# Optimization experiments

Measured on AMD Instinct MI355X. Metric: run time of the kernel, lower is better.

Reference implementation:

```python
import jax, jax.numpy as jnp
import numpy as np

D_MODEL = 512
NUM_HEADS = 8
BATCH = 2
SEQ = 2048


def setup_inputs() -> dict:
    key = jax.random.key(0)
    ks = jax.random.split(key, 10)
    H = D_MODEL * NUM_HEADS  # concat width = 4096
    scale_in = 1.0 / np.sqrt(D_MODEL)
    scale_h = 1.0 / np.sqrt(H)
    inp = {
        "input_data": jax.random.normal(ks[0], (BATCH, SEQ, D_MODEL), dtype=jnp.float32),
        # causal mask, broadcastable to [n, h, q, k]; masked_fill where mask == 0
        "mask": jnp.tril(jnp.ones((SEQ, SEQ), dtype=jnp.int32))[None, None, :, :],
        "Wq": jax.random.normal(ks[1], (D_MODEL, H), dtype=jnp.float32) * scale_in,
        "bq": jnp.zeros((H,), dtype=jnp.float32),
        "Wk": jax.random.normal(ks[2], (D_MODEL, H), dtype=jnp.float32) * scale_in,
        "bk": jnp.zeros((H,), dtype=jnp.float32),
        "Wv": jax.random.normal(ks[3], (D_MODEL, H), dtype=jnp.float32) * scale_in,
        "bv": jnp.zeros((H,), dtype=jnp.float32),
        "Wo": jax.random.normal(ks[4], (H, D_MODEL), dtype=jnp.float32) * scale_h,
        "bo": jnp.zeros((D_MODEL,), dtype=jnp.float32),
    }
    return inp


def reference(input_data, mask, Wq, bq, Wk, bk, Wv, bv, Wo, bo):
    n, s, d_model = input_data.shape
    H = Wq.shape[1] // d_model  # num_heads; per-head dim == d_model in this module
    q = (input_data @ Wq + bq).reshape(n, s, H, d_model)
    k = (input_data @ Wk + bk).reshape(n, s, H, d_model)
    v = (input_data @ Wv + bv).reshape(n, s, H, d_model)
    scores = jnp.einsum('nqhd,nkhd->nhqk', q, k) / jnp.sqrt(jnp.float32(d_model))
    scores = jnp.where(mask == 0, jnp.float32(-1e9), scores)
    weights = jax.nn.softmax(scores, axis=-1)
    # Faithful to source: contracts weights over BOTH k and q axes (source quirk)
    output = jnp.einsum('nhkq,nvhd->nvhd', weights, v)
    concat = output.reshape(n, s, H * d_model)
    return concat @ Wo + bo
```

## Files before the change

kernel.cpp:

```cpp
#include <hip/hip_runtime.h>


#define DM 512
#define HC 4096
#define SEQF 2048.0f

typedef short bf16x8 __attribute__((ext_vector_type(8)));
typedef float f32x4 __attribute__((ext_vector_type(4)));

#define LDR 40

__device__ __forceinline__ void split2(float x, ushort& h, ushort& l) {
    unsigned b = __float_as_uint(x);
    h = (ushort)(b >> 16);
    float hf = __uint_as_float((unsigned)(h) << 16);
    l = (ushort)(__float_as_uint(x - hf) >> 16);
}

template <int ROWS>
__device__ __forceinline__ void stage_f32(const float* __restrict__ src, int ld, int row0,
                                          int k0, ushort* Hh, ushort* Hl, int tid) {
    const int r   = (ROWS == 128) ? (tid >> 1) : (tid >> 2);
    const int co  = (ROWS == 128) ? ((tid & 1) * 16) : ((tid & 3) * 8);
    const int NF4 = (ROWS == 128) ? 4 : 2;
    const float* p = src + (size_t)(row0 + r) * ld + k0 + co;
#pragma unroll
    for (int c = 0; c < NF4; ++c) {
        float4 v = *reinterpret_cast<const float4*>(p + c * 4);
        ushort4 uh, ul;
        split2(v.x, uh.x, ul.x);
        split2(v.y, uh.y, ul.y);
        split2(v.z, uh.z, ul.z);
        split2(v.w, uh.w, ul.w);
        *reinterpret_cast<ushort4*>(&Hh[r * LDR + co + c * 4]) = uh;
        *reinterpret_cast<ushort4*>(&Hl[r * LDR + co + c * 4]) = ul;
    }
}

template <int ROWS>
__device__ __forceinline__ void stage_bf16(const ushort* __restrict__ srcH,
                                           const ushort* __restrict__ srcL, int ld, int row0,
                                           int k0, ushort* Hh, ushort* Hl, int tid) {
    const int r   = (ROWS == 128) ? (tid >> 1) : (tid >> 2);
    const int co  = (ROWS == 128) ? ((tid & 1) * 16) : ((tid & 3) * 8);
    const int NI4 = (ROWS == 128) ? 2 : 1;
    const size_t off = (size_t)(row0 + r) * ld + k0 + co;
#pragma unroll
    for (int c = 0; c < NI4; ++c) {
        *reinterpret_cast<int4*>(&Hh[r * LDR + co + c * 8]) =
            *reinterpret_cast<const int4*>(&srcH[off + c * 8]);
        *reinterpret_cast<int4*>(&Hl[r * LDR + co + c * 8]) =
            *reinterpret_cast<const int4*>(&srcL[off + c * 8]);
    }
}

__global__ __launch_bounds__(256) void prep_wo(const float* __restrict__ Wo,
                                               const float* __restrict__ bv,
                                               ushort* __restrict__ WoTh,
                                               ushort* __restrict__ WoTl,
                                               float* __restrict__ cvec) {
    __shared__ float T[64][65];
    const int bj = blockIdx.x;
    const int bn = blockIdx.y;
    const int tid = threadIdx.x;
    {
        const int r = tid >> 2, c16 = (tid & 3) * 16;
        const float* p = Wo + (size_t)(bj * 64 + r) * DM + bn * 64 + c16;
#pragma unroll
        for (int c = 0; c < 4; ++c) {
            float4 v = *reinterpret_cast<const float4*>(p + c * 4);
            T[r][c16 + c * 4 + 0] = v.x;
            T[r][c16 + c * 4 + 1] = v.y;
            T[r][c16 + c * 4 + 2] = v.z;
            T[r][c16 + c * 4 + 3] = v.w;
        }
    }
    __syncthreads();
    {
        const int rn = tid >> 2, c16 = (tid & 3) * 16;
        const size_t off = (size_t)(bn * 64 + rn) * HC + bj * 64 + c16;
#pragma unroll
        for (int q = 0; q < 4; ++q) {
            ushort4 uh, ul;
            split2(T[c16 + q * 4 + 0][rn], uh.x, ul.x);
            split2(T[c16 + q * 4 + 1][rn], uh.y, ul.y);
            split2(T[c16 + q * 4 + 2][rn], uh.z, ul.z);
            split2(T[c16 + q * 4 + 3][rn], uh.w, ul.w);
            *reinterpret_cast<ushort4*>(&WoTh[off + q * 4]) = uh;
            *reinterpret_cast<ushort4*>(&WoTl[off + q * 4]) = ul;
        }
    }
    if (tid < 64) {
        float s = 0.f;
#pragma unroll 8
        for (int j = 0; j < 64; ++j) s = fmaf(bv[bj * 64 + j], T[j][tid], s);
        atomicAdd(&cvec[bn * 64 + tid], SEQF * s);
    }
}

__global__ __launch_bounds__(256) void gemm_wcT(const ushort* __restrict__ WoTh,
                                                const ushort* __restrict__ WoTl,
                                                const float* __restrict__ Wv,
                                                float* __restrict__ WcT) {
    __shared__ ushort Ah[128 * LDR], Al[128 * LDR], Bh[128 * LDR], Bl[128 * LDR];
    const int d = blockIdx.x;
    const int lin = (d & 7) * 32 + (d >> 3);
    const int kc = lin >> 4, mt = (lin >> 2) & 3, nt = lin & 3;
    const int a0 = mt * 128, b0 = nt * 128, kbase = kc * 256;
    const int tid = threadIdx.x, wave = tid >> 6, lane = tid & 63;
    const int wm = (wave >> 1) * 64, wn = (wave & 1) * 64;
    const int fr = lane & 15, fs = (lane >> 4) * 8;

    f32x4 acc[4][4] = {};
    for (int t = 0; t < 8; ++t) {
        const int k0 = kbase + t * 32;
        stage_bf16<128>(WoTh, WoTl, HC, a0, k0, Ah, Al, tid);
        stage_f32<128>(Wv, HC, b0, k0, Bh, Bl, tid);
        __syncthreads();
        bf16x8 afh[4], afl[4], bfh[4], bfl[4];
#pragma unroll
        for (int f = 0; f < 4; ++f) {
            const int ai = (wm + f * 16 + fr) * LDR + fs;
            afh[f] = *reinterpret_cast<const bf16x8*>(&Ah[ai]);
            afl[f] = *reinterpret_cast<const bf16x8*>(&Al[ai]);
            const int bi = (wn + f * 16 + fr) * LDR + fs;
            bfh[f] = *reinterpret_cast<const bf16x8*>(&Bh[bi]);
            bfl[f] = *reinterpret_cast<const bf16x8*>(&Bl[bi]);
        }
#pragma unroll
        for (int f = 0; f < 4; ++f)
#pragma unroll
            for (int g = 0; g < 4; ++g) {
                acc[f][g] = __builtin_amdgcn_mfma_f32_16x16x32_bf16(afh[f], bfh[g], acc[f][g], 0, 0, 0);
                acc[f][g] = __builtin_amdgcn_mfma_f32_16x16x32_bf16(afh[f], bfl[g], acc[f][g], 0, 0, 0);
                acc[f][g] = __builtin_amdgcn_mfma_f32_16x16x32_bf16(afl[f], bfh[g], acc[f][g], 0, 0, 0);
            }
        __syncthreads();
    }
#pragma unroll
    for (int f = 0; f < 4; ++f)
#pragma unroll
        for (int g = 0; g < 4; ++g)
#pragma unroll
            for (int q = 0; q < 4; ++q) {
                const int row = a0 + wm + f * 16 + (lane >> 4) * 4 + q;
                const int col = b0 + wn + g * 16 + (lane & 15);
                atomicAdd(&WcT[(size_t)row * DM + col], SEQF * acc[f][g][q]);
            }
}

__global__ __launch_bounds__(256) void prep_wct(const float* __restrict__ WcT,
                                                ushort* __restrict__ WcTh,
                                                ushort* __restrict__ WcTl) {
    const int i = blockIdx.x * 256 + threadIdx.x;
    const float4 v = reinterpret_cast<const float4*>(WcT)[i];
    ushort4 uh, ul;
    split2(v.x, uh.x, ul.x);
    split2(v.y, uh.y, ul.y);
    split2(v.z, uh.z, ul.z);
    split2(v.w, uh.w, ul.w);
    reinterpret_cast<ushort4*>(WcTh)[i] = uh;
    reinterpret_cast<ushort4*>(WcTl)[i] = ul;
}

__global__ __launch_bounds__(256) void gemm_out(const float* __restrict__ X,
                                                const ushort* __restrict__ WcTh,
                                                const ushort* __restrict__ WcTl,
                                                const float* __restrict__ cvec,
                                                const float* __restrict__ bo,
                                                float* __restrict__ out) {
    __shared__ ushort Ah[64 * LDR], Al[64 * LDR], Bh[128 * LDR], Bl[128 * LDR];
    const int d = blockIdx.x;
    const int lin = (d & 7) * 32 + (d >> 3);
    const int nt = lin >> 6, mt = lin & 63;
    const int a0 = mt * 64, b0 = nt * 128;
    const int tid = threadIdx.x, wave = tid >> 6, lane = tid & 63;
    const int wm = (wave >> 1) * 32, wn = (wave & 1) * 64;
    const int fr = lane & 15, fs = (lane >> 4) * 8;

    f32x4 acc[2][4] = {};
    for (int t = 0; t < 16; ++t) {
        const int k0 = t * 32;
        stage_f32<64>(X, DM, a0, k0, Ah, Al, tid);
        stage_bf16<128>(WcTh, WcTl, DM, b0, k0, Bh, Bl, tid);
        __syncthreads();
        bf16x8 afh[2], afl[2], bfh[4], bfl[4];
#pragma unroll
        for (int f = 0; f < 2; ++f) {
            const int ai = (wm + f * 16 + fr) * LDR + fs;
            afh[f] = *reinterpret_cast<const bf16x8*>(&Ah[ai]);
            afl[f] = *reinterpret_cast<const bf16x8*>(&Al[ai]);
        }
#pragma unroll
        for (int g = 0; g < 4; ++g) {
            const int bi = (wn + g * 16 + fr) * LDR + fs;
            bfh[g] = *reinterpret_cast<const bf16x8*>(&Bh[bi]);
            bfl[g] = *reinterpret_cast<const bf16x8*>(&Bl[bi]);
        }
#pragma unroll
        for (int f = 0; f < 2; ++f)
#pragma unroll
            for (int g = 0; g < 4; ++g) {
                acc[f][g] = __builtin_amdgcn_mfma_f32_16x16x32_bf16(afh[f], bfh[g], acc[f][g], 0, 0, 0);
                acc[f][g] = __builtin_amdgcn_mfma_f32_16x16x32_bf16(afh[f], bfl[g], acc[f][g], 0, 0, 0);
                acc[f][g] = __builtin_amdgcn_mfma_f32_16x16x32_bf16(afl[f], bfh[g], acc[f][g], 0, 0, 0);
            }
        __syncthreads();
    }
#pragma unroll
    for (int g = 0; g < 4; ++g) {
        const int n = b0 + wn + g * 16 + (lane & 15);
        const float cb = cvec[n] + bo[n];
#pragma unroll
        for (int f = 0; f < 2; ++f)
#pragma unroll
            for (int q = 0; q < 4; ++q) {
                const int m = a0 + wm + f * 16 + (lane >> 4) * 4 + q;
                out[(size_t)m * DM + n] = acc[f][g][q] + cb;
            }
    }
}

extern "C" void kernel_launch(void* const* d_in, const int* in_sizes, int n_in,
                              void* d_out, int out_size, void* d_ws, size_t ws_size,
                              hipStream_t stream) {
    const float* input = (const float*)d_in[0];
    const float* Wv    = (const float*)d_in[6];
    const float* bv    = (const float*)d_in[7];
    const float* Wo    = (const float*)d_in[8];
    const float* bo    = (const float*)d_in[9];
    float* out = (float*)d_out;

    ushort* WoTh = (ushort*)d_ws;
    ushort* WoTl = WoTh + (size_t)DM * HC;
    float*  WcT  = (float*)(WoTl + (size_t)DM * HC);
    ushort* WcTh = (ushort*)(WcT + DM * DM);
    ushort* WcTl = WcTh + DM * DM;
    float*  cvec = (float*)(WcTl + DM * DM);

    hipMemsetAsync(WcT, 0, (size_t)DM * DM * 8 + DM * 4, stream);

    prep_wo<<<dim3(64, 8), 256, 0, stream>>>(Wo, bv, WoTh, WoTl, cvec);
    gemm_wcT<<<256, 256, 0, stream>>>(WoTh, WoTl, Wv, WcT);
    prep_wct<<<256, 256, 0, stream>>>(WcT, WcTh, WcTl);
    gemm_out<<<256, 256, 0, stream>>>(input, WcTh, WcTl, cvec, bo, out);
}
```

Before: 156.6 us.

## Use 64x64 tiles in both GEMMs and fold WcT split into gemm_out staging

Both GEMMs move to 64x64 block tiles with one 16-row strip per wave, doubling the grid to 512 blocks for better CU occupancy. gemm_wcT now uses split-K over 8 chunks of 512 instead of 16 chunks of 256, which halves the atomic traffic per output. The separate prep_wct kernel is removed, and gemm_out splits WcT into hi/lo bf16 on the fly while staging. This saves one launch and a round trip through memory, at the cost of redundant split work and less register-level reuse per wave.

```diff
diff --git a/kernel.cpp b/kernel.cpp
--- a/kernel.cpp
+++ b/kernel.cpp
@@ -4,54 +4,44 @@
 #define DM 512
 #define HC 4096
 #define SEQF 2048.0f
+#define LDR 40
 
 typedef short bf16x8 __attribute__((ext_vector_type(8)));
 typedef float f32x4 __attribute__((ext_vector_type(4)));
 
-#define LDR 40
-
 __device__ __forceinline__ void split2(float x, ushort& h, ushort& l) {
     unsigned b = __float_as_uint(x);
     h = (ushort)(b >> 16);
-    float hf = __uint_as_float((unsigned)(h) << 16);
+    float hf = __uint_as_float((unsigned)h << 16);
     l = (ushort)(__float_as_uint(x - hf) >> 16);
 }
 
-template <int ROWS>
-__device__ __forceinline__ void stage_f32(const float* __restrict__ src, int ld, int row0,
-                                          int k0, ushort* Hh, ushort* Hl, int tid) {
-    const int r   = (ROWS == 128) ? (tid >> 1) : (tid >> 2);
-    const int co  = (ROWS == 128) ? ((tid & 1) * 16) : ((tid & 3) * 8);
-    const int NF4 = (ROWS == 128) ? 4 : 2;
+__device__ __forceinline__ void stage64_f32(const float* __restrict__ src, int ld,
+                                            int row0, int k0, ushort* Hh, ushort* Hl,
+                                            int tid) {
+    const int r = tid >> 2, co = (tid & 3) * 8;
     const float* p = src + (size_t)(row0 + r) * ld + k0 + co;
-#pragma unroll
-    for (int c = 0; c < NF4; ++c) {
-        float4 v = *reinterpret_cast<const float4*>(p + c * 4);
-        ushort4 uh, ul;
-        split2(v.x, uh.x, ul.x);
-        split2(v.y, uh.y, ul.y);
-        split2(v.z, uh.z, ul.z);
-        split2(v.w, uh.w, ul.w);
-        *reinterpret_cast<ushort4*>(&Hh[r * LDR + co + c * 4]) = uh;
-        *reinterpret_cast<ushort4*>(&Hl[r * LDR + co + c * 4]) = ul;
-    }
+    const float4 v0 = *reinterpret_cast<const float4*>(p);
+    const float4 v1 = *reinterpret_cast<const float4*>(p + 4);
+    ushort4 h0, l0, h1, l1;
+    split2(v0.x, h0.x, l0.x); split2(v0.y, h0.y, l0.y);
+    split2(v0.z, h0.z, l0.z); split2(v0.w, h0.w, l0.w);
+    split2(v1.x, h1.x, l1.x); split2(v1.y, h1.y, l1.y);
+    split2(v1.z, h1.z, l1.z); split2(v1.w, h1.w, l1.w);
+    *reinterpret_cast<ushort4*>(&Hh[r * LDR + co])     = h0;
+    *reinterpret_cast<ushort4*>(&Hh[r * LDR + co + 4]) = h1;
+    *reinterpret_cast<ushort4*>(&Hl[r * LDR + co])     = l0;
+    *reinterpret_cast<ushort4*>(&Hl[r * LDR + co + 4]) = l1;
 }
 
-template <int ROWS>
-__device__ __forceinline__ void stage_bf16(const ushort* __restrict__ srcH,
-                                           const ushort* __restrict__ srcL, int ld, int row0,
-                                           int k0, ushort* Hh, ushort* Hl, int tid) {
-    const int r   = (ROWS == 128) ? (tid >> 1) : (tid >> 2);
-    const int co  = (ROWS == 128) ? ((tid & 1) * 16) : ((tid & 3) * 8);
-    const int NI4 = (ROWS == 128) ? 2 : 1;
+__device__ __forceinline__ void stage64_bf16(const ushort* __restrict__ sh,
+                                             const ushort* __restrict__ sl, int ld,
+                                             int row0, int k0, ushort* Hh, ushort* Hl,
+                                             int tid) {
+    const int r = tid >> 2, co = (tid & 3) * 8;
     const size_t off = (size_t)(row0 + r) * ld + k0 + co;
-#pragma unroll
-    for (int c = 0; c < NI4; ++c) {
-        *reinterpret_cast<int4*>(&Hh[r * LDR + co + c * 8]) =
-            *reinterpret_cast<const int4*>(&srcH[off + c * 8]);
-        *reinterpret_cast<int4*>(&Hl[r * LDR + co + c * 8]) =
-            *reinterpret_cast<const int4*>(&srcL[off + c * 8]);
-    }
+    *reinterpret_cast<int4*>(&Hh[r * LDR + co]) = *reinterpret_cast<const int4*>(&sh[off]);
+    *reinterpret_cast<int4*>(&Hl[r * LDR + co]) = *reinterpret_cast<const int4*>(&sl[off]);
 }
 
 __global__ __launch_bounds__(256) void prep_wo(const float* __restrict__ Wo,
@@ -102,122 +92,87 @@
                                                 const ushort* __restrict__ WoTl,
                                                 const float* __restrict__ Wv,
                                                 float* __restrict__ WcT) {
-    __shared__ ushort Ah[128 * LDR], Al[128 * LDR], Bh[128 * LDR], Bl[128 * LDR];
+    __shared__ ushort Ah[64 * LDR], Al[64 * LDR], Bh[64 * LDR], Bl[64 * LDR];
     const int d = blockIdx.x;
-    const int lin = (d & 7) * 32 + (d >> 3);
-    const int kc = lin >> 4, mt = (lin >> 2) & 3, nt = lin & 3;
-    const int a0 = mt * 128, b0 = nt * 128, kbase = kc * 256;
+    const int lin = (d & 7) * 64 + (d >> 3);
+    const int kc = lin >> 6, tile = lin & 63;
+    const int nt = tile >> 3, it = tile & 7;
+    const int a0 = nt * 64, b0 = it * 64, kb = kc * 512;
     const int tid = threadIdx.x, wave = tid >> 6, lane = tid & 63;
-    const int wm = (wave >> 1) * 64, wn = (wave & 1) * 64;
-    const int fr = lane & 15, fs = (lane >> 4) * 8;
+    const int wm = wave * 16, fr = lane & 15, fs = (lane >> 4) * 8;
 
-    f32x4 acc[4][4] = {};
-    for (int t = 0; t < 8; ++t) {
-        const int k0 = kbase + t * 32;
-        stage_bf16<128>(WoTh, WoTl, HC, a0, k0, Ah, Al, tid);
-        stage_f32<128>(Wv, HC, b0, k0, Bh, Bl, tid);
+    f32x4 acc[4] = {};
+    for (int t = 0; t < 16; ++t) {
+        const int k0 = kb + t * 32;
+        stage64_bf16(WoTh, WoTl, HC, a0, k0, Ah, Al, tid);
+        stage64_f32(Wv, HC, b0, k0, Bh, Bl, tid);
         __syncthreads();
-        bf16x8 afh[4], afl[4], bfh[4], bfl[4];
+        const int ai = (wm + fr) * LDR + fs;
+        const bf16x8 ah = *reinterpret_cast<const bf16x8*>(&Ah[ai]);
+        const bf16x8 al = *reinterpret_cast<const bf16x8*>(&Al[ai]);
 #pragma unroll
-        for (int f = 0; f < 4; ++f) {
-            const int ai = (wm + f * 16 + fr) * LDR + fs;
-            afh[f] = *reinterpret_cast<const bf16x8*>(&Ah[ai]);
-            afl[f] = *reinterpret_cast<const bf16x8*>(&Al[ai]);
-            const int bi = (wn + f * 16 + fr) * LDR + fs;
-            bfh[f] = *reinterpret_cast<const bf16x8*>(&Bh[bi]);
-            bfl[f] = *reinterpret_cast<const bf16x8*>(&Bl[bi]);
+        for (int g = 0; g < 4; ++g) {
+            const int bi = (g * 16 + fr) * LDR + fs;
+            const bf16x8 bh = *reinterpret_cast<const bf16x8*>(&Bh[bi]);
+            const bf16x8 bl = *reinterpret_cast<const bf16x8*>(&Bl[bi]);
+            acc[g] = __builtin_amdgcn_mfma_f32_16x16x32_bf16(ah, bh, acc[g], 0, 0, 0);
+            acc[g] = __builtin_amdgcn_mfma_f32_16x16x32_bf16(ah, bl, acc[g], 0, 0, 0);
+            acc[g] = __builtin_amdgcn_mfma_f32_16x16x32_bf16(al, bh, acc[g], 0, 0, 0);
         }
-#pragma unroll
-        for (int f = 0; f < 4; ++f)
-#pragma unroll
-            for (int g = 0; g < 4; ++g) {
-                acc[f][g] = __builtin_amdgcn_mfma_f32_16x16x32_bf16(afh[f], bfh[g], acc[f][g], 0, 0, 0);
-                acc[f][g] = __builtin_amdgcn_mfma_f32_16x16x32_bf16(afh[f], bfl[g], acc[f][g], 0, 0, 0);
-                acc[f][g] = __builtin_amdgcn_mfma_f32_16x16x32_bf16(afl[f], bfh[g], acc[f][g], 0, 0, 0);
-            }
         __syncthreads();
     }
 #pragma unroll
-    for (int f = 0; f < 4; ++f)
+    for (int g = 0; g < 4; ++g)
 #pragma unroll
-        for (int g = 0; g < 4; ++g)
-#pragma unroll
-            for (int q = 0; q < 4; ++q) {
-                const int row = a0 + wm + f * 16 + (lane >> 4) * 4 + q;
-                const int col = b0 + wn + g * 16 + (lane & 15);
-                atomicAdd(&WcT[(size_t)row * DM + col], SEQF * acc[f][g][q]);
-            }
-}
-
-__global__ __launch_bounds__(256) void prep_wct(const float* __restrict__ WcT,
-                                                ushort* __restrict__ WcTh,
-                                                ushort* __restrict__ WcTl) {
-    const int i = blockIdx.x * 256 + threadIdx.x;
-    const float4 v = reinterpret_cast<const float4*>(WcT)[i];
-    ushort4 uh, ul;
-    split2(v.x, uh.x, ul.x);
-    split2(v.y, uh.y, ul.y);
-    split2(v.z, uh.z, ul.z);
-    split2(v.w, uh.w, ul.w);
-    reinterpret_cast<ushort4*>(WcTh)[i] = uh;
-    reinterpret_cast<ushort4*>(WcTl)[i] = ul;
+        for (int q = 0; q < 4; ++q) {
+            const int row = a0 + wm + (lane >> 4) * 4 + q;
+            const int col = b0 + g * 16 + (lane & 15);
+            atomicAdd(&WcT[(size_t)row * DM + col], SEQF * acc[g][q]);
+        }
 }
 
 __global__ __launch_bounds__(256) void gemm_out(const float* __restrict__ X,
-                                                const ushort* __restrict__ WcTh,
-                                                const ushort* __restrict__ WcTl,
+                                                const float* __restrict__ WcT,
                                                 const float* __restrict__ cvec,
                                                 const float* __restrict__ bo,
                                                 float* __restrict__ out) {
-    __shared__ ushort Ah[64 * LDR], Al[64 * LDR], Bh[128 * LDR], Bl[128 * LDR];
+    __shared__ ushort Ah[64 * LDR], Al[64 * LDR], Bh[64 * LDR], Bl[64 * LDR];
     const int d = blockIdx.x;
-    const int lin = (d & 7) * 32 + (d >> 3);
-    const int nt = lin >> 6, mt = lin & 63;
-    const int a0 = mt * 64, b0 = nt * 128;
+    const int lin = (d & 7) * 64 + (d >> 3);
+    const int mt = lin >> 3, nt = lin & 7;
+    const int a0 = mt * 64, b0 = nt * 64;
     const int tid = threadIdx.x, wave = tid >> 6, lane = tid & 63;
-    const int wm = (wave >> 1) * 32, wn = (wave & 1) * 64;
-    const int fr = lane & 15, fs = (lane >> 4) * 8;
+    const int wm = wave * 16, fr = lane & 15, fs = (lane >> 4) * 8;
 
-    f32x4 acc[2][4] = {};
+    f32x4 acc[4] = {};
     for (int t = 0; t < 16; ++t) {
         const int k0 = t * 32;
-        stage_f32<64>(X, DM, a0, k0, Ah, Al, tid);
-        stage_bf16<128>(WcTh, WcTl, DM, b0, k0, Bh, Bl, tid);
+        stage64_f32(X, DM, a0, k0, Ah, Al, tid);
+        stage64_f32(WcT, DM, b0, k0, Bh, Bl, tid);
         __syncthreads();
-        bf16x8 afh[2], afl[2], bfh[4], bfl[4];
-#pragma unroll
-        for (int f = 0; f < 2; ++f) {
-            const int ai = (wm + f * 16 + fr) * LDR + fs;
-            afh[f] = *reinterpret_cast<const bf16x8*>(&Ah[ai]);
-            afl[f] = *reinterpret_cast<const bf16x8*>(&Al[ai]);
-        }
+        const int ai = (wm + fr) * LDR + fs;
+        const bf16x8 ah = *reinterpret_cast<const bf16x8*>(&Ah[ai]);
+        const bf16x8 al = *reinterpret_cast<const bf16x8*>(&Al[ai]);
 #pragma unroll
         for (int g = 0; g < 4; ++g) {
-            const int bi = (wn + g * 16 + fr) * LDR + fs;
-            bfh[g] = *reinterpret_cast<const bf16x8*>(&Bh[bi]);
-            bfl[g] = *reinterpret_cast<const bf16x8*>(&Bl[bi]);
+            const int bi = (g * 16 + fr) * LDR + fs;
+            const bf16x8 bh = *reinterpret_cast<const bf16x8*>(&Bh[bi]);
+            const bf16x8 bl = *reinterpret_cast<const bf16x8*>(&Bl[bi]);
+            acc[g] = __builtin_amdgcn_mfma_f32_16x16x32_bf16(ah, bh, acc[g], 0, 0, 0);
+            acc[g] = __builtin_amdgcn_mfma_f32_16x16x32_bf16(ah, bl, acc[g], 0, 0, 0);
+            acc[g] = __builtin_amdgcn_mfma_f32_16x16x32_bf16(al, bh, acc[g], 0, 0, 0);
         }
-#pragma unroll
-        for (int f = 0; f < 2; ++f)
-#pragma unroll
-            for (int g = 0; g < 4; ++g) {
-                acc[f][g] = __builtin_amdgcn_mfma_f32_16x16x32_bf16(afh[f], bfh[g], acc[f][g], 0, 0, 0);
-                acc[f][g] = __builtin_amdgcn_mfma_f32_16x16x32_bf16(afh[f], bfl[g], acc[f][g], 0, 0, 0);
-                acc[f][g] = __builtin_amdgcn_mfma_f32_16x16x32_bf16(afl[f], bfh[g], acc[f][g], 0, 0, 0);
-            }
         __syncthreads();
     }
 #pragma unroll
     for (int g = 0; g < 4; ++g) {
-        const int n = b0 + wn + g * 16 + (lane & 15);
+        const int n = b0 + g * 16 + (lane & 15);
         const float cb = cvec[n] + bo[n];
 #pragma unroll
-        for (int f = 0; f < 2; ++f)
-#pragma unroll
-            for (int q = 0; q < 4; ++q) {
-                const int m = a0 + wm + f * 16 + (lane >> 4) * 4 + q;
-                out[(size_t)m * DM + n] = acc[f][g][q] + cb;
-            }
+        for (int q = 0; q < 4; ++q) {
+            const int m = a0 + wm + (lane >> 4) * 4 + q;
+            out[(size_t)m * DM + n] = acc[g][q] + cb;
+        }
     }
 }
 
@@ -234,14 +189,11 @@
     ushort* WoTh = (ushort*)d_ws;
     ushort* WoTl = WoTh + (size_t)DM * HC;
     float*  WcT  = (float*)(WoTl + (size_t)DM * HC);
-    ushort* WcTh = (ushort*)(WcT + DM * DM);
-    ushort* WcTl = WcTh + DM * DM;
-    float*  cvec = (float*)(WcTl + DM * DM);
+    float*  cvec = WcT + (size_t)DM * DM;
 
-    hipMemsetAsync(WcT, 0, (size_t)DM * DM * 8 + DM * 4, stream);
+    hipMemsetAsync(WcT, 0, (size_t)DM * DM * 4 + DM * 4, stream);
 
     prep_wo<<<dim3(64, 8), 256, 0, stream>>>(Wo, bv, WoTh, WoTl, cvec);
-    gemm_wcT<<<256, 256, 0, stream>>>(WoTh, WoTl, Wv, WcT);
-    prep_wct<<<256, 256, 0, stream>>>(WcT, WcTh, WcTl);
-    gemm_out<<<256, 256, 0, stream>>>(input, WcTh, WcTl, cvec, bo, out);
+    gemm_wcT<<<512, 256, 0, stream>>>(WoTh, WoTl, Wv, WcT);
+    gemm_out<<<512, 256, 0, stream>>>(input, WcT, cvec, bo, out);
 }
```

After: 154.4 us. Within noise of the previous version (-1.4%).
